# Performance work log

Hardware: AMD Instinct MI355X
Metric: run time of the kernel (lower is better)

The kernel has to match this reference:

```python
import jax, jax.numpy as jnp
import numpy as np

B = 64       # batch
D = 768      # embed dim
NH = 12      # heads
HD = 64      # head dim
P = 16       # patch size
IMG = 224
G = IMG // P # 14 patches per side
N = G * G    # 196 patch tokens
T = N + 1    # +CLS
M = 4 * D    # MLP hidden 3072
LE = 9       # early blocks (8 prefix + last_early)
LL = 3       # late ragged blocks
NC = 1000    # classes
TAU = 0.9    # ATS CDF keep threshold
SCALE = 1.0 / np.sqrt(float(HD))


def setup_inputs() -> dict:
    keys = iter(jax.random.split(jax.random.key(0), 48))
    def w(shape):
        return jax.random.normal(next(keys), shape, jnp.float32) * 0.02
    def layer_params(L, prefix, d):
        d[prefix + "ln1_g"] = jnp.ones((L, D)); d[prefix + "ln1_b"] = jnp.zeros((L, D))
        d[prefix + "qkv_w"] = w((L, D, 3 * D)); d[prefix + "qkv_b"] = jnp.zeros((L, 3 * D))
        d[prefix + "proj_w"] = w((L, D, D)); d[prefix + "proj_b"] = jnp.zeros((L, D))
        d[prefix + "ln2_g"] = jnp.ones((L, D)); d[prefix + "ln2_b"] = jnp.zeros((L, D))
        d[prefix + "fc1_w"] = w((L, D, M)); d[prefix + "fc1_b"] = jnp.zeros((L, M))
        d[prefix + "fc2_w"] = w((L, M, D)); d[prefix + "fc2_b"] = jnp.zeros((L, D))
    inp = {}
    inp["images"] = jax.random.normal(next(keys), (B, 3, IMG, IMG), jnp.float32)
    inp["patch_w"] = w((D, 3, P, P)); inp["patch_b"] = jnp.zeros((D,))
    inp["cls_token"] = w((1, 1, D)); inp["pos_embed"] = w((1, T, D))
    layer_params(LE, "e_", inp)
    layer_params(LL, "l_", inp)
    inp["norm_g"] = jnp.ones((D,)); inp["norm_b"] = jnp.zeros((D,))
    inp["head_w"] = w((D, NC)); inp["head_b"] = jnp.zeros((NC,))
    return inp


def _ln(x, g, b):
    m = x.mean(-1, keepdims=True)
    v = ((x - m) ** 2).mean(-1, keepdims=True)
    return (x - m) * jax.lax.rsqrt(v + 1e-6) * g + b


def _block(x, p, i, key_mask=None):
    # Pre-LN ViT block; returns (x, post-softmax attention weights).
    Bb, Tt, _ = x.shape
    y = _ln(x, p["ln1_g"][i], p["ln1_b"][i])
    qkv = (y @ p["qkv_w"][i] + p["qkv_b"][i]).reshape(Bb, Tt, 3, NH, HD)
    q, k, v = jnp.moveaxis(qkv, 2, 0)                      # each [B,T,H,HD]
    logits = jnp.einsum("bqhd,bkhd->bhqk", q, k) * SCALE
    if key_mask is not None:
        # ragged attention: dropped tokens never act as keys (== packed varlen attn)
        logits = jnp.where(key_mask[:, None, None, :], logits, -1e9)
    a = jax.nn.softmax(logits, axis=-1)
    o = jnp.einsum("bhqk,bkhd->bqhd", a, v).reshape(Bb, Tt, D)
    x = x + o @ p["proj_w"][i] + p["proj_b"][i]
    y = _ln(x, p["ln2_g"][i], p["ln2_b"][i])
    y = jax.nn.gelu(y @ p["fc1_w"][i] + p["fc1_b"][i], approximate=False)
    x = x + y @ p["fc2_w"][i] + p["fc2_b"][i]
    return x, a


def reference(images, patch_w, patch_b, cls_token, pos_embed,
              e_ln1_g, e_ln1_b, e_qkv_w, e_qkv_b, e_proj_w, e_proj_b,
              e_ln2_g, e_ln2_b, e_fc1_w, e_fc1_b, e_fc2_w, e_fc2_b,
              l_ln1_g, l_ln1_b, l_qkv_w, l_qkv_b, l_proj_w, l_proj_b,
              l_ln2_g, l_ln2_b, l_fc1_w, l_fc1_b, l_fc2_w, l_fc2_b,
              norm_g, norm_b, head_w, head_b):
    loc = dict(locals())
    e = {k[2:]: v for k, v in loc.items() if k.startswith("e_")}
    l = {k[2:]: v for k, v in loc.items() if k.startswith("l_")}

    # front: patch embed (stride-P conv as einsum) + CLS + pos
    xi = images.reshape(B, 3, G, P, G, P)
    tok = jnp.einsum("bchpwq,dcpq->bhwd", xi, patch_w).reshape(B, N, D) + patch_b
    x = jnp.concatenate([jnp.broadcast_to(cls_token, (B, 1, D)), tok], axis=1) + pos_embed

    # early prefix + last_early (capture attn)
    attn = None
    for i in range(LE):
        x, attn = _block(x, e, i)

    # ATS importance scores: CLS attention (head-avg) * token feature norm, normalized
    cls_attn = attn.mean(axis=1)[:, 0, 1:]                 # [B,N]
    raw = cls_attn * jnp.linalg.norm(x[:, 1:, :], axis=-1)
    s = raw / (raw.sum(-1, keepdims=True) + 1e-12)

    # CDF mask: keep highest-scoring tokens until cumulative importance reaches TAU
    order = jnp.argsort(-s, axis=-1)
    cdf = jnp.cumsum(jnp.take_along_axis(s, order, axis=-1), axis=-1)
    keep_sorted = (cdf <= TAU).at[:, 0].set(True)          # always keep best token
    mask = jnp.zeros((B, N), bool).at[jnp.arange(B)[:, None], order].set(keep_sorted)
    key_mask = jnp.concatenate([jnp.ones((B, 1), bool), mask], axis=1)  # CLS kept

    # ragged late blocks (masked attention == packed variable-length attention)
    for i in range(LL):
        x, _ = _block(x, l, i, key_mask)

    # back: gather CLS (position 0 == cu_seqlens offsets), norm, head
    cls = _ln(x[:, 0, :], norm_g, norm_b)
    return cls @ head_w + head_b
```

## Files before the change

kernel.cpp:

```cpp
#include <hip/hip_runtime.h>
#include <hip/hip_bf16.h>
#include <math.h>

typedef __attribute__((ext_vector_type(8))) short s16x8;
typedef __attribute__((ext_vector_type(4))) short s16x4;
typedef __attribute__((ext_vector_type(4))) float f32x4;

#define MP 12672
#define MREAL 12608
#define PROWS 12544
#define SCALE 0.125f

__device__ __forceinline__ float gelu_exact(float z) {
    return 0.5f * z * (1.f + erff(z * 0.7071067811865475f));
}

__global__ void zero_pad_rows(float* __restrict__ x) {
    int r = MREAL + blockIdx.x;
    x[(size_t)r * 768 + threadIdx.x] = 0.f;
}

__global__ void set_cls(const float* __restrict__ cls, const float* __restrict__ pos,
                        float* __restrict__ x) {
    int b = blockIdx.x, t = threadIdx.x;
    x[(size_t)b * 197 * 768 + t] = cls[t] + pos[t];
}

__global__ void cast_pw(const float* __restrict__ w, __hip_bfloat16* __restrict__ o, int n) {
    int i = blockIdx.x * 256 + threadIdx.x;
    if (i < n) o[i] = __float2bfloat16(w[i]);
}

__global__ void im2col_kernel(const float* __restrict__ img, __hip_bfloat16* __restrict__ P) {
    int row = blockIdx.x;
    int t = threadIdx.x;
    if (row >= PROWS) {
        for (int k = t; k < 768; k += 256) P[(size_t)row * 768 + k] = __float2bfloat16(0.f);
        return;
    }
    int b = row / 196, n = row % 196;
    int gh = n / 14, gw = n % 14;
    for (int k = t; k < 768; k += 256) {
        int c = k >> 8, rem = k & 255, p = rem >> 4, q = rem & 15;
        float v = img[((size_t)(b * 3 + c) * 224 + (gh * 16 + p)) * 224 + gw * 16 + q];
        P[(size_t)row * 768 + k] = __float2bfloat16(v);
    }
}

__global__ void transpose_cast_all(const float* __restrict__ qkvw,
                                   const float* __restrict__ projw,
                                   const float* __restrict__ fc1w,
                                   const float* __restrict__ fc2w,
                                   __hip_bfloat16* __restrict__ wt) {
    __shared__ float tile[32][33];
    int bid = blockIdx.x;
    const float* W; __hip_bfloat16* D; int K, N, tn;
    if (bid < 1728) { W = qkvw; D = wt; K = 768; N = 2304; tn = 72; }
    else if (bid < 2304) { bid -= 1728; W = projw; D = wt + 1769472; K = 768; N = 768; tn = 24; }
    else if (bid < 4608) { bid -= 2304; W = fc1w; D = wt + 2359296; K = 768; N = 3072; tn = 96; }
    else { bid -= 4608; W = fc2w; D = wt + 4718592; K = 3072; N = 768; tn = 24; }
    int n0 = (bid % tn) * 32, k0 = (bid / tn) * 32;
    int tx = threadIdx.x, ty = threadIdx.y;
    #pragma unroll
    for (int i = 0; i < 4; ++i)
        tile[ty + i * 8][tx] = W[(size_t)(k0 + ty + i * 8) * N + n0 + tx];
    __syncthreads();
    #pragma unroll
    for (int i = 0; i < 4; ++i)
        D[(size_t)(n0 + ty + i * 8) * K + k0 + tx] = __float2bfloat16(tile[tx][ty + i * 8]);
}

__global__ void ln_bf16_w(const float* __restrict__ x, const float* __restrict__ g,
                          const float* __restrict__ bia, __hip_bfloat16* __restrict__ y) {
    int row = blockIdx.x * 4 + (threadIdx.x >> 6);
    int lane = threadIdx.x & 63;
    const float* xr = x + (size_t)row * 768;
    f32x4 v[3];
    float s = 0.f, s2 = 0.f;
    #pragma unroll
    for (int i = 0; i < 3; ++i) {
        v[i] = *(const f32x4*)&xr[lane * 4 + i * 256];
        #pragma unroll
        for (int j = 0; j < 4; ++j) { s += v[i][j]; s2 += v[i][j] * v[i][j]; }
    }
    #pragma unroll
    for (int off = 1; off < 64; off <<= 1) { s += __shfl_xor(s, off); s2 += __shfl_xor(s2, off); }
    float mean = s * (1.f / 768.f);
    float var = s2 * (1.f / 768.f) - mean * mean;
    float rs = rsqrtf(var + 1e-6f);
    #pragma unroll
    for (int i = 0; i < 3; ++i) {
        int c = lane * 4 + i * 256;
        f32x4 gg = *(const f32x4*)&g[c];
        f32x4 bb = *(const f32x4*)&bia[c];
        s16x4 o;
        #pragma unroll
        for (int j = 0; j < 4; ++j) {
            __hip_bfloat16 hb = __float2bfloat16((v[i][j] - mean) * rs * gg[j] + bb[j]);
            o[j] = *(short*)&hb;
        }
        *(s16x4*)&y[(size_t)row * 768 + c] = o;
    }
}

__global__ void ln_cls_t(const float* __restrict__ x, const float* __restrict__ g,
                         const float* __restrict__ bia, float* __restrict__ At) {
    int b = blockIdx.x;
    const float* xr = x + (size_t)b * 197 * 768;
    int t = threadIdx.x;
    float v[3];
    float s = 0.f, s2 = 0.f;
    #pragma unroll
    for (int i = 0; i < 3; ++i) { v[i] = xr[t + 256 * i]; s += v[i]; s2 += v[i] * v[i]; }
    __shared__ float r1[256], r2[256];
    r1[t] = s; r2[t] = s2; __syncthreads();
    for (int off = 128; off > 0; off >>= 1) {
        if (t < off) { r1[t] += r1[t + off]; r2[t] += r2[t + off]; }
        __syncthreads();
    }
    float mean = r1[0] * (1.f / 768.f);
    float var = r2[0] * (1.f / 768.f) - mean * mean;
    float rs = rsqrtf(var + 1e-6f);
    #pragma unroll
    for (int i = 0; i < 3; ++i) {
        int c = t + 256 * i;
        At[(size_t)c * 64 + b] = (v[i] - mean) * rs * g[c] + bia[c];
    }
}

template <int EPI>
__global__ __launch_bounds__(256)
void gemm_mfma(const __hip_bfloat16* __restrict__ A,
               const __hip_bfloat16* __restrict__ Bt,
               const float* __restrict__ bias,
               const float* res, float* Cf, __hip_bfloat16* Cb,
               const float* __restrict__ pos,
               int Nc, int K) {
    __shared__ short As[8192];
    __shared__ short Bs[8192];
    int tid = threadIdx.x;
    int lane = tid & 63, w = tid >> 6;
    int wr = w >> 1, wc = w & 1;
    int nwg = gridDim.x * gridDim.y;
    int bid = blockIdx.y * gridDim.x + blockIdx.x;
    int xcd = bid & 7, idx = bid >> 3;
    int qq = nwg >> 3, rr = nwg & 7;
    int swz = (xcd < rr ? xcd * (qq + 1) : rr * (qq + 1) + (xcd - rr) * qq) + idx;
    int bm = (swz / gridDim.x) * 128, bn = (swz % gridDim.x) * 128;
    int l15 = lane & 15, lh = lane >> 4;
    f32x4 acc[4][4] = {};
    for (int k0 = 0; k0 < K; k0 += 64) {
        #pragma unroll
        for (int q = 0; q < 4; ++q) {
            int S = (w * 4 + q) * 64 + lane;
            int row = S >> 3;
            int c = (S & 7) ^ (row & 7);
            const __hip_bfloat16* sA = A + (size_t)(bm + row) * K + (k0 + c * 8);
            const __hip_bfloat16* sB = Bt + (size_t)(bn + row) * K + (k0 + c * 8);
            __builtin_amdgcn_global_load_lds(
                (const __attribute__((address_space(1))) void*)sA,
                (__attribute__((address_space(3))) void*)&As[(w * 4 + q) * 512], 16, 0, 0);
            __builtin_amdgcn_global_load_lds(
                (const __attribute__((address_space(1))) void*)sB,
                (__attribute__((address_space(3))) void*)&Bs[(w * 4 + q) * 512], 16, 0, 0);
        }
        __syncthreads();
        #pragma unroll
        for (int ks = 0; ks < 2; ++ks) {
            s16x8 av[4], bv[4];
            int c = ks * 4 + lh;
            #pragma unroll
            for (int i = 0; i < 4; ++i) {
                int ra = wr * 64 + i * 16 + l15;
                av[i] = *(const s16x8*)&As[(ra * 8 + (c ^ (ra & 7))) * 8];
                int rb = wc * 64 + i * 16 + l15;
                bv[i] = *(const s16x8*)&Bs[(rb * 8 + (c ^ (rb & 7))) * 8];
            }
            #pragma unroll
            for (int i = 0; i < 4; ++i)
                #pragma unroll
                for (int j = 0; j < 4; ++j)
                    acc[i][j] = __builtin_amdgcn_mfma_f32_16x16x32_bf16(av[i], bv[j], acc[i][j], 0, 0, 0);
        }
        __syncthreads();
    }
    #pragma unroll
    for (int i = 0; i < 4; ++i) {
        #pragma unroll
        for (int j = 0; j < 4; ++j) {
            int colg = bn + wc * 64 + j * 16 + l15;
            float bcol = bias[colg];
            #pragma unroll
            for (int r = 0; r < 4; ++r) {
                int rowg = bm + wr * 64 + i * 16 + lh * 4 + r;
                float v = acc[i][j][r] + bcol;
                if (EPI == 0) {
                    Cf[(size_t)rowg * Nc + colg] = v;
                } else if (EPI == 1) {
                    Cf[(size_t)rowg * Nc + colg] = v + res[(size_t)rowg * Nc + colg];
                } else if (EPI == 2) {
                    Cb[(size_t)rowg * Nc + colg] = __float2bfloat16(gelu_exact(v));
                } else if (EPI == 4) {
                    Cb[(size_t)rowg * Nc + colg] = __float2bfloat16(v);
                } else {
                    if (rowg < PROWS) {
                        int b = rowg / 196, n = rowg % 196;
                        Cf[((size_t)b * 197 + 1 + n) * 768 + colg] = v + pos[(size_t)(1 + n) * 768 + colg];
                    }
                }
            }
        }
    }
}

__global__ __launch_bounds__(512)
void attn_mfma(const __hip_bfloat16* __restrict__ qkvp, const int* __restrict__ key_mask,
               __hip_bfloat16* __restrict__ o, float* __restrict__ cls_row,
               int useMask, int saveCls) {
    int h = blockIdx.x, b = blockIdx.y;
    __shared__ short Kl[224 * 64];
    __shared__ short Vt[64 * 256];
    __shared__ short Pl[8][4096];
    __shared__ unsigned mword[7];
    const short* qkv = (const short*)qkvp;
    int t = threadIdx.x;

    if (t < 7) {
        unsigned wb = 0;
        for (int j = 0; j < 32; ++j) {
            int k = t * 32 + j;
            int bit = (k < 197) ? (useMask ? (key_mask[b * 197 + k] != 0) : 1) : 0;
            wb |= (unsigned)bit << j;
        }
        mword[t] = wb;
    }
    {
        int c = t & 7, kr0 = t >> 3;
        for (int it = 0; it < 4; ++it) {
            int krow = kr0 + it * 64;
            if (krow < 224) {
                s16x8 v;
                if (krow < 197) {
                    v = *(const s16x8*)(qkv + (size_t)(b * 197 + krow) * 2304 + 768 + h * 64 + c * 8);
                } else {
                    #pragma unroll
                    for (int j = 0; j < 8; ++j) v[j] = 0;
                }
                *(s16x8*)&Kl[(krow * 8 + (c ^ (krow & 7))) * 8] = v;
            }
        }
    }
    {
        int d = t & 63, cb = t >> 6;
        for (int it = 0; it < 4; ++it) {
            int c = cb + it * 8;
            s16x8 v;
            #pragma unroll
            for (int j = 0; j < 8; ++j) {
                int k = c * 8 + j;
                v[j] = (k < 197) ? qkv[(size_t)(b * 197 + k) * 2304 + 1536 + h * 64 + d] : (short)0;
            }
            *(s16x8*)&Vt[(d * 32 + (c ^ (d & 7))) * 8] = v;
        }
    }
    __syncthreads();

    int w = t >> 6, lane = t & 63;
    int l15 = lane & 15, lh = lane >> 4;
    unsigned mw[7];
    #pragma unroll
    for (int i = 0; i < 7; ++i) mw[i] = mword[i];
    short* Pw = &Pl[w][0];

    for (int qf = w; qf < 13; qf += 8) {
        int qbase = qf * 16;
        int q = qbase + l15;
        const short* qptr = qkv + (size_t)(b * 197 + q) * 2304 + h * 64;
        s16x8 bq0 = *(const s16x8*)(qptr + lh * 8);
        s16x8 bq1 = *(const s16x8*)(qptr + 32 + lh * 8);

        f32x4 sacc[14];
        #pragma unroll
        for (int mf = 0; mf < 14; ++mf) sacc[mf] = (f32x4){0.f, 0.f, 0.f, 0.f};
        #pragma unroll
        for (int mf = 0; mf < 14; ++mf) {
            int row = mf * 16 + l15;
            s16x8 a0 = *(const s16x8*)&Kl[(row * 8 + (lh ^ (row & 7))) * 8];
            s16x8 a1 = *(const s16x8*)&Kl[(row * 8 + ((4 + lh) ^ (row & 7))) * 8];
            sacc[mf] = __builtin_amdgcn_mfma_f32_16x16x32_bf16(a0, bq0, sacc[mf], 0, 0, 0);
            sacc[mf] = __builtin_amdgcn_mfma_f32_16x16x32_bf16(a1, bq1, sacc[mf], 0, 0, 0);
        }
        float m = -1e30f;
        #pragma unroll
        for (int mf = 0; mf < 14; ++mf) {
            #pragma unroll
            for (int r = 0; r < 4; ++r) {
                int k = mf * 16 + lh * 4 + r;
                int keep = (mw[k >> 5] >> (k & 31)) & 1;
                float lg = keep ? sacc[mf][r] * SCALE : -1e30f;
                sacc[mf][r] = lg;
                m = fmaxf(m, lg);
            }
        }
        m = fmaxf(m, __shfl_xor(m, 16));
        m = fmaxf(m, __shfl_xor(m, 32));
        float sum = 0.f;
        #pragma unroll
        for (int mf = 0; mf < 14; ++mf) {
            #pragma unroll
            for (int r = 0; r < 4; ++r) {
                float p = expf(sacc[mf][r] - m);
                sum += p;
                sacc[mf][r] = p;
            }
        }
        sum += __shfl_xor(sum, 16);
        sum += __shfl_xor(sum, 32);
        float inv = 1.f / sum;
        if (saveCls && qf == 0 && l15 == 0) {
            #pragma unroll
            for (int mf = 0; mf < 14; ++mf)
                #pragma unroll
                for (int r = 0; r < 4; ++r) {
                    int k = mf * 16 + lh * 4 + r;
                    if (k < 197) cls_row[((size_t)b * 12 + h) * 197 + k] = sacc[mf][r] * inv;
                }
        }
        #pragma unroll
        for (int mf = 0; mf < 14; ++mf) {
            s16x4 pk;
            #pragma unroll
            for (int r = 0; r < 4; ++r) {
                __hip_bfloat16 hb = __float2bfloat16(sacc[mf][r] * inv);
                pk[r] = *(short*)&hb;
            }
            int slot = l15 * 32 + ((mf * 2 + (lh >> 1)) ^ (l15 & 7));
            *(s16x4*)&Pw[slot * 8 + (lh & 1) * 4] = pk;
        }
        f32x4 oacc[4];
        #pragma unroll
        for (int nf = 0; nf < 4; ++nf) oacc[nf] = (f32x4){0.f, 0.f, 0.f, 0.f};
        #pragma unroll
        for (int ks = 0; ks < 7; ++ks) {
            int c = ks * 4 + lh;
            s16x8 pa = *(const s16x8*)&Pw[(l15 * 32 + (c ^ (l15 & 7))) * 8];
            #pragma unroll
            for (int nf = 0; nf < 4; ++nf) {
                int d = nf * 16 + l15;
                s16x8 bv = *(const s16x8*)&Vt[(d * 32 + (c ^ (d & 7))) * 8];
                oacc[nf] = __builtin_amdgcn_mfma_f32_16x16x32_bf16(pa, bv, oacc[nf], 0, 0, 0);
            }
        }
        #pragma unroll
        for (int nf = 0; nf < 4; ++nf) {
            #pragma unroll
            for (int r = 0; r < 4; ++r) {
                int q2 = qbase + lh * 4 + r;
                if (q2 < 197)
                    o[(size_t)(b * 197 + q2) * 768 + h * 64 + nf * 16 + l15] =
                        __float2bfloat16(oacc[nf][r]);
            }
        }
    }
}

__global__ void cls_scores(const float* __restrict__ x, const float* __restrict__ cls_row,
                           float* __restrict__ raw) {
    int bn = blockIdx.x;
    int b = bn / 196, n = bn % 196;
    const float* xr = x + ((size_t)b * 197 + 1 + n) * 768;
    int t = threadIdx.x;
    float s2 = 0.f;
    for (int c = t; c < 768; c += 256) { float v = xr[c]; s2 += v * v; }
    __shared__ float r[256];
    r[t] = s2; __syncthreads();
    for (int off = 128; off > 0; off >>= 1) {
        if (t < off) r[t] += r[t + off];
        __syncthreads();
    }
    if (t == 0) {
        float ca = 0.f;
        for (int h = 0; h < 12; ++h) ca += cls_row[((size_t)b * 12 + h) * 197 + 1 + n];
        raw[bn] = (ca * (1.f / 12.f)) * sqrtf(r[0]);
    }
}

__global__ void ats_mask_kernel(const float* __restrict__ raw, int* __restrict__ key_mask) {
    int b = blockIdx.x, t = threadIdx.x;
    __shared__ float s[196];
    __shared__ float ssorted[196];
    __shared__ int keep[196];
    __shared__ float red[256];
    float v = (t < 196) ? raw[b * 196 + t] : 0.f;
    red[t] = v; __syncthreads();
    for (int off = 128; off > 0; off >>= 1) {
        if (t < off) red[t] += red[t + off];
        __syncthreads();
    }
    float total = red[0];
    if (t < 196) s[t] = v / (total + 1e-12f);
    __syncthreads();
    int rk = 0;
    if (t < 196) {
        float mys = s[t];
        for (int j = 0; j < 196; ++j) {
            float sj = s[j];
            rk += (sj > mys) || (sj == mys && j < t);
        }
        ssorted[rk] = mys;
    }
    __syncthreads();
    if (t == 0) {
        float c = 0.f;
        for (int k = 0; k < 196; ++k) {
            c += ssorted[k];
            keep[k] = (c <= 0.9f) || (k == 0);
        }
    }
    __syncthreads();
    if (t == 0) key_mask[b * 197] = 1;
    if (t < 196) key_mask[b * 197 + 1 + t] = keep[rk];
}

__global__ void gemm_head_t(const float* __restrict__ At, const float* __restrict__ W,
                            const float* __restrict__ bias, float* __restrict__ out) {
    int col = blockIdx.x;
    int t = threadIdx.x;
    int row = t & 63, part = t >> 6;
    float acc = 0.f;
    for (int i = 0; i < 192; ++i) {
        int k = part * 192 + i;
        acc += At[(size_t)k * 64 + row] * W[(size_t)k * 1000 + col];
    }
    __shared__ float red[256];
    red[t] = acc; __syncthreads();
    if (part == 0)
        out[(size_t)row * 1000 + col] = red[row] + red[64 + row] + red[128 + row] + red[192 + row]
                                        + bias[col];
}

extern "C" void kernel_launch(void* const* d_in, const int* in_sizes, int n_in,
                              void* d_out, int out_size, void* d_ws, size_t ws_size,
                              hipStream_t stream) {
    const float* images  = (const float*)d_in[0];
    const float* patch_w = (const float*)d_in[1];
    const float* patch_b = (const float*)d_in[2];
    const float* cls_tok = (const float*)d_in[3];
    const float* pos_emb = (const float*)d_in[4];
    const float* e_p[12]; const float* l_p[12];
    for (int i = 0; i < 12; ++i) e_p[i] = (const float*)d_in[5 + i];
    for (int i = 0; i < 12; ++i) l_p[i] = (const float*)d_in[17 + i];
    const float* norm_g = (const float*)d_in[29];
    const float* norm_b = (const float*)d_in[30];
    const float* head_w = (const float*)d_in[31];
    const float* head_b = (const float*)d_in[32];
    float* out = (float*)d_out;

    float* ws = (float*)d_ws;
    size_t off = 0;
    float* x = ws + off; off += (size_t)MP * 768;
    __hip_bfloat16* ybf = (__hip_bfloat16*)(ws + off); off += (size_t)MP * 768 / 2;
    float* qh = ws + off; off += (size_t)MP * 3072;
    __hip_bfloat16* qbf = (__hip_bfloat16*)qh;
    __hip_bfloat16* P = (__hip_bfloat16*)qh;
    __hip_bfloat16* hbf = (__hip_bfloat16*)qh;
    __hip_bfloat16* wt = (__hip_bfloat16*)(ws + off); off += (size_t)7077888 / 2;
    __hip_bfloat16* pwb = (__hip_bfloat16*)(ws + off); off += (size_t)589824 / 2;
    float* clsrow = ws + off; off += (size_t)64 * 12 * 197;
    float* raw = ws + off; off += (size_t)64 * 196;
    float* At = ws + off; off += (size_t)768 * 64;
    int* kmask = (int*)(ws + off); off += (size_t)64 * 197;

    __hip_bfloat16* wt_qkv  = wt;
    __hip_bfloat16* wt_proj = wt_qkv + (size_t)2304 * 768;
    __hip_bfloat16* wt_fc1  = wt_proj + (size_t)768 * 768;
    __hip_bfloat16* wt_fc2  = wt_fc1 + (size_t)3072 * 768;

    zero_pad_rows<<<64, 768, 0, stream>>>(x);
    set_cls<<<64, 768, 0, stream>>>(cls_tok, pos_emb, x);
    cast_pw<<<2304, 256, 0, stream>>>(patch_w, pwb, 589824);
    im2col_kernel<<<MP, 256, 0, stream>>>(images, P);
    gemm_mfma<3><<<dim3(6, 99), 256, 0, stream>>>(P, pwb, patch_b, nullptr, x, nullptr,
                                                  pos_emb, 768, 768);

    for (int blk = 0; blk < 12; ++blk) {
        bool early = blk < 9;
        int i = early ? blk : blk - 9;
        const float* const* p = early ? e_p : l_p;
        const float* ln1g = p[0] + (size_t)i * 768;
        const float* ln1b = p[1] + (size_t)i * 768;
        const float* qkvw = p[2] + (size_t)i * 768 * 2304;
        const float* qkvb = p[3] + (size_t)i * 2304;
        const float* projw = p[4] + (size_t)i * 768 * 768;
        const float* projb = p[5] + (size_t)i * 768;
        const float* ln2g = p[6] + (size_t)i * 768;
        const float* ln2b = p[7] + (size_t)i * 768;
        const float* fc1w = p[8] + (size_t)i * 768 * 3072;
        const float* fc1b = p[9] + (size_t)i * 3072;
        const float* fc2w = p[10] + (size_t)i * 3072 * 768;
        const float* fc2b = p[11] + (size_t)i * 768;
        int useMask = early ? 0 : 1;
        int saveCls = (early && i == 8) ? 1 : 0;

        transpose_cast_all<<<6912, dim3(32, 8), 0, stream>>>(qkvw, projw, fc1w, fc2w, wt);

        ln_bf16_w<<<MP / 4, 256, 0, stream>>>(x, ln1g, ln1b, ybf);
        gemm_mfma<4><<<dim3(18, 99), 256, 0, stream>>>(ybf, wt_qkv, qkvb, nullptr, nullptr, qbf,
                                                       nullptr, 2304, 768);
        attn_mfma<<<dim3(12, 64), 512, 0, stream>>>(qbf, kmask, ybf, clsrow, useMask, saveCls);
        gemm_mfma<1><<<dim3(6, 99), 256, 0, stream>>>(ybf, wt_proj, projb, x, x, nullptr,
                                                      nullptr, 768, 768);
        ln_bf16_w<<<MP / 4, 256, 0, stream>>>(x, ln2g, ln2b, ybf);
        gemm_mfma<2><<<dim3(24, 99), 256, 0, stream>>>(ybf, wt_fc1, fc1b, nullptr, nullptr, hbf,
                                                       nullptr, 3072, 768);
        gemm_mfma<1><<<dim3(6, 99), 256, 0, stream>>>(hbf, wt_fc2, fc2b, x, x, nullptr,
                                                      nullptr, 768, 3072);

        if (saveCls) {
            cls_scores<<<12544, 256, 0, stream>>>(x, clsrow, raw);
            ats_mask_kernel<<<64, 256, 0, stream>>>(raw, kmask);
        }
    }

    ln_cls_t<<<64, 256, 0, stream>>>(x, norm_g, norm_b, At);
    gemm_head_t<<<1000, 256, 0, stream>>>(At, head_w, head_b, out);
}
```

Before: 4.565 ms.

## Add 256x128 tile 8-wave MFMA GEMM for QKV and FC1 with triple buffering

Adds a new 512-thread GEMM kernel that computes 256x128 output tiles with eight waves. It uses a three-slot LDS ring filled by global_load_lds with XOR swizzling, XCD-aware block remapping, and setprio around the MFMA bursts. The kernel replaces the 128-row-tile GEMM for the QKV and FC1 projections. The padded row count grows from 12672 to 12800 so M divides by 256, which means the other GEMMs, LayerNorm and zero-padding now process a few more padded rows. The goal is more operand reuse per tile and better overlap of loads with MFMA, at the cost of higher LDS use per block and lower occupancy.

Result: slower. 4.675 ms (+2.4%).

```diff
diff --git a/kernel.cpp b/kernel.cpp
--- a/kernel.cpp
+++ b/kernel.cpp
@@ -6,7 +6,7 @@
 typedef __attribute__((ext_vector_type(4))) short s16x4;
 typedef __attribute__((ext_vector_type(4))) float f32x4;
 
-#define MP 12672
+#define MP 12800
 #define MREAL 12608
 #define PROWS 12544
 #define SCALE 0.125f
@@ -213,6 +213,99 @@
     }
 }
 
+template <int EPI>
+__global__ __launch_bounds__(512)
+void gemm_mfma8(const __hip_bfloat16* __restrict__ A,
+                const __hip_bfloat16* __restrict__ Bt,
+                const float* __restrict__ bias,
+                __hip_bfloat16* __restrict__ Cb,
+                int Nc, int K) {
+    __shared__ short As[3 * 16384];
+    __shared__ short Bs[3 * 8192];
+    int tid = threadIdx.x;
+    int lane = tid & 63, w = tid >> 6;
+    int wr = w >> 1, wc = w & 1;
+    int nwg = gridDim.x * gridDim.y;
+    int bid = blockIdx.y * gridDim.x + blockIdx.x;
+    int xcd = bid & 7, idx = bid >> 3;
+    int qq = nwg >> 3, rr = nwg & 7;
+    int swz = (xcd < rr ? xcd * (qq + 1) : rr * (qq + 1) + (xcd - rr) * qq) + idx;
+    int bm = (swz / gridDim.x) * 256, bn = (swz % gridDim.x) * 128;
+    int l15 = lane & 15, lh = lane >> 4;
+    int NT = K >> 6;
+
+    auto STAGE_A = [&](int t, int q) {
+        int slot = t % 3;
+        int S = q * 512 + tid;
+        int row = S >> 3, c = (S & 7) ^ (row & 7);
+        __builtin_amdgcn_global_load_lds(
+            (const __attribute__((address_space(1))) void*)(A + (size_t)(bm + row) * K + t * 64 + c * 8),
+            (__attribute__((address_space(3))) void*)&As[slot * 16384 + S * 8], 16, 0, 0);
+    };
+    auto STAGE_B = [&](int t, int q) {
+        int slot = t % 3;
+        int S = q * 512 + tid;
+        int row = S >> 3, c = (S & 7) ^ (row & 7);
+        __builtin_amdgcn_global_load_lds(
+            (const __attribute__((address_space(1))) void*)(Bt + (size_t)(bn + row) * K + t * 64 + c * 8),
+            (__attribute__((address_space(3))) void*)&Bs[slot * 8192 + S * 8], 16, 0, 0);
+    };
+
+    f32x4 acc[4][4] = {};
+    STAGE_A(0, 0); STAGE_A(0, 1); STAGE_A(0, 2); STAGE_A(0, 3); STAGE_B(0, 0); STAGE_B(0, 1);
+    STAGE_A(1, 0); STAGE_A(1, 1); STAGE_A(1, 2); STAGE_A(1, 3); STAGE_B(1, 0); STAGE_B(1, 1);
+
+    for (int t = 0; t < NT; ++t) {
+        if (t + 1 < NT) { asm volatile("s_waitcnt vmcnt(6)" ::: "memory"); }
+        else            { asm volatile("s_waitcnt vmcnt(0)" ::: "memory"); }
+        __builtin_amdgcn_s_barrier();
+        const short* Ab = &As[(t % 3) * 16384];
+        const short* Bb = &Bs[(t % 3) * 8192];
+        bool pf = (t + 2 < NT);
+        #pragma unroll
+        for (int ks = 0; ks < 2; ++ks) {
+            s16x8 av[4], bv[4];
+            int c = ks * 4 + lh;
+            #pragma unroll
+            for (int i = 0; i < 4; ++i) {
+                int ra = wr * 64 + i * 16 + l15;
+                av[i] = *(const s16x8*)&Ab[(ra * 8 + (c ^ (ra & 7))) * 8];
+                int rb = wc * 64 + i * 16 + l15;
+                bv[i] = *(const s16x8*)&Bb[(rb * 8 + (c ^ (rb & 7))) * 8];
+            }
+            if (pf) {
+                if (ks == 0) { STAGE_A(t + 2, 0); STAGE_A(t + 2, 1); STAGE_A(t + 2, 2); }
+                else         { STAGE_A(t + 2, 3); STAGE_B(t + 2, 0); STAGE_B(t + 2, 1); }
+            }
+            __builtin_amdgcn_s_setprio(1);
+            #pragma unroll
+            for (int i = 0; i < 4; ++i)
+                #pragma unroll
+                for (int j = 0; j < 4; ++j)
+                    acc[i][j] = __builtin_amdgcn_mfma_f32_16x16x32_bf16(av[i], bv[j], acc[i][j], 0, 0, 0);
+            __builtin_amdgcn_s_setprio(0);
+        }
+    }
+    #pragma unroll
+    for (int i = 0; i < 4; ++i) {
+        #pragma unroll
+        for (int j = 0; j < 4; ++j) {
+            int colg = bn + wc * 64 + j * 16 + l15;
+            float bcol = bias[colg];
+            #pragma unroll
+            for (int r = 0; r < 4; ++r) {
+                int rowg = bm + wr * 64 + i * 16 + lh * 4 + r;
+                float v = acc[i][j][r] + bcol;
+                if (EPI == 2) {
+                    Cb[(size_t)rowg * Nc + colg] = __float2bfloat16(gelu_exact(v));
+                } else {
+                    Cb[(size_t)rowg * Nc + colg] = __float2bfloat16(v);
+                }
+            }
+        }
+    }
+}
+
 __global__ __launch_bounds__(512)
 void attn_mfma(const __hip_bfloat16* __restrict__ qkvp, const int* __restrict__ key_mask,
                __hip_bfloat16* __restrict__ o, float* __restrict__ cls_row,
@@ -476,12 +569,12 @@
     __hip_bfloat16* wt_fc1  = wt_proj + (size_t)768 * 768;
     __hip_bfloat16* wt_fc2  = wt_fc1 + (size_t)3072 * 768;
 
-    zero_pad_rows<<<64, 768, 0, stream>>>(x);
+    zero_pad_rows<<<192, 768, 0, stream>>>(x);
     set_cls<<<64, 768, 0, stream>>>(cls_tok, pos_emb, x);
     cast_pw<<<2304, 256, 0, stream>>>(patch_w, pwb, 589824);
     im2col_kernel<<<MP, 256, 0, stream>>>(images, P);
-    gemm_mfma<3><<<dim3(6, 99), 256, 0, stream>>>(P, pwb, patch_b, nullptr, x, nullptr,
-                                                  pos_emb, 768, 768);
+    gemm_mfma<3><<<dim3(6, 100), 256, 0, stream>>>(P, pwb, patch_b, nullptr, x, nullptr,
+                                                   pos_emb, 768, 768);
 
     for (int blk = 0; blk < 12; ++blk) {
         bool early = blk < 9;
@@ -505,16 +598,14 @@
         transpose_cast_all<<<6912, dim3(32, 8), 0, stream>>>(qkvw, projw, fc1w, fc2w, wt);
 
         ln_bf16_w<<<MP / 4, 256, 0, stream>>>(x, ln1g, ln1b, ybf);
-        gemm_mfma<4><<<dim3(18, 99), 256, 0, stream>>>(ybf, wt_qkv, qkvb, nullptr, nullptr, qbf,
-                                                       nullptr, 2304, 768);
+        gemm_mfma8<4><<<dim3(18, 50), 512, 0, stream>>>(ybf, wt_qkv, qkvb, qbf, 2304, 768);
         attn_mfma<<<dim3(12, 64), 512, 0, stream>>>(qbf, kmask, ybf, clsrow, useMask, saveCls);
-        gemm_mfma<1><<<dim3(6, 99), 256, 0, stream>>>(ybf, wt_proj, projb, x, x, nullptr,
-                                                      nullptr, 768, 768);
+        gemm_mfma<1><<<dim3(6, 100), 256, 0, stream>>>(ybf, wt_proj, projb, x, x, nullptr,
+                                                       nullptr, 768, 768);
         ln_bf16_w<<<MP / 4, 256, 0, stream>>>(x, ln2g, ln2b, ybf);
-        gemm_mfma<2><<<dim3(24, 99), 256, 0, stream>>>(ybf, wt_fc1, fc1b, nullptr, nullptr, hbf,
-                                                       nullptr, 3072, 768);
-        gemm_mfma<1><<<dim3(6, 99), 256, 0, stream>>>(hbf, wt_fc2, fc2b, x, x, nullptr,
-                                                      nullptr, 768, 3072);
+        gemm_mfma8<2><<<dim3(24, 50), 512, 0, stream>>>(ybf, wt_fc1, fc1b, hbf, 3072, 768);
+        gemm_mfma<1><<<dim3(6, 100), 256, 0, stream>>>(hbf, wt_fc2, fc2b, x, x, nullptr,
+                                                       nullptr, 768, 3072);
 
         if (saveCls) {
             cls_scores<<<12544, 256, 0, stream>>>(x, clsrow, raw);
```
